# Kernel tuning notes

Hardware: AMD Instinct MI355X
Metric: run time of the kernel (lower is better)

The kernel has to match this reference:

```python
import jax, jax.numpy as jnp
import numpy as np

N, IN, D, H, C, G = 50000, 128, 64, 4, 10, 64
E_RAND = 800000
NEG_SLOPE = 0.2  # DGL GATConv default LeakyReLU slope


def setup_inputs() -> dict:
    key = jax.random.key(0)
    ks = jax.random.split(key, 20)
    h = jax.random.normal(ks[0], (N, IN), jnp.float32)
    # random edges + self-loops so every dst has at least one in-edge
    src = jnp.concatenate([jax.random.randint(ks[1], (E_RAND,), 0, N), jnp.arange(N)]).astype(jnp.int32)
    dst = jnp.concatenate([jax.random.randint(ks[2], (E_RAND,), 0, N), jnp.arange(N)]).astype(jnp.int32)
    graph_id = jnp.sort(jax.random.randint(ks[3], (N,), 0, G)).astype(jnp.int32)
    w = lambda k, s: jax.random.normal(k, s, jnp.float32) * 0.1
    return {
        "h": h, "src": src, "dst": dst, "graph_id": graph_id,
        "W0": w(ks[4], (IN, H * D)),    "al0": w(ks[5], (H, D)), "ar0": w(ks[6], (H, D)),
        "W1": w(ks[7], (H * D, H * D)), "al1": w(ks[8], (H, D)), "ar1": w(ks[9], (H, D)),
        "W2": w(ks[10], (H * D, H * D)), "al2": w(ks[11], (H, D)), "ar2": w(ks[12], (H, D)),
        "W3": w(ks[13], (H * D, D)),    "al3": w(ks[14], (1, D)), "ar3": w(ks[15], (1, D)),
        "fc1_w": w(ks[16], (D, D)), "fc1_b": jnp.zeros((D,), jnp.float32),
        "fc2_w": w(ks[17], (D, C)), "fc2_b": jnp.zeros((C,), jnp.float32),
    }


def gat_layer(x, W, al, ar, src, dst):
    """DGL GATConv: z=xW; e=LeakyReLU(a_l.z_src + a_r.z_dst); softmax over in-edges of dst; out=sum alpha*z_src."""
    nh, nd = al.shape
    z = (x @ W).reshape(N, nh, nd)                      # [N,H,D]
    el = jnp.sum(z * al, axis=-1)                       # [N,H]
    er = jnp.sum(z * ar, axis=-1)                       # [N,H]
    e = jax.nn.leaky_relu(el[src] + er[dst], NEG_SLOPE)  # [E,H]
    m = jax.ops.segment_max(e, dst, num_segments=N)     # per-dst max (stable softmax)
    ex = jnp.exp(e - m[dst])
    den = jax.ops.segment_sum(ex, dst, num_segments=N)
    alpha = ex / den[dst]                               # [E,H]
    msg = alpha[:, :, None] * z[src]                    # [E,H,D]
    return jax.ops.segment_sum(msg, dst, num_segments=N)  # [N,H,D]


def reference(h, src, dst, graph_id, W0, al0, ar0, W1, al1, ar1, W2, al2, ar2,
              W3, al3, ar3, fc1_w, fc1_b, fc2_w, fc2_b):
    x = jax.nn.relu(gat_layer(h, W0, al0, ar0, src, dst).reshape(N, -1))
    x = jax.nn.relu(gat_layer(x, W1, al1, ar1, src, dst).reshape(N, -1))
    x = jax.nn.relu(gat_layer(x, W2, al2, ar2, src, dst).reshape(N, -1))
    x = jax.nn.relu(gat_layer(x, W3, al3, ar3, src, dst).reshape(N, -1))  # [N,D] (1 head)
    # AvgPooling: mean node features per graph
    counts = jax.ops.segment_sum(jnp.ones((N,), x.dtype), graph_id, num_segments=G)
    pooled = jax.ops.segment_sum(x, graph_id, num_segments=G) / jnp.maximum(counts, 1.0)[:, None]
    y = jax.nn.elu(pooled @ fc1_w + fc1_b)
    y = y @ fc2_w + fc2_b
    return jax.nn.log_softmax(y, axis=0)  # original applies log_softmax over dim=0
```

## Files before the change

kernel.cpp:

```cpp
#include <hip/hip_runtime.h>
#include <hip/hip_bf16.h>
#include <math.h>

#define NN 50000
#define IN_F 128
#define DD 64
#define HH 4
#define CC 10
#define GG 64
#define NEG_SLOPE 0.2f

typedef __attribute__((ext_vector_type(8))) short bf16x8;
typedef __attribute__((ext_vector_type(4))) float f32x4;
typedef __attribute__((ext_vector_type(4))) unsigned short u16x4;

__device__ inline ushort f2bf(float f) {
    unsigned u = __float_as_uint(f);
    unsigned r = (u + 0x7fffu + ((u >> 16) & 1u)) >> 16;
    return (ushort)r;
}
__device__ inline float bf2f(ushort b) { return __uint_as_float(((unsigned)b) << 16); }

__device__ inline float wave_max(float v) {
#pragma unroll
    for (int o = 32; o > 0; o >>= 1) v = fmaxf(v, __shfl_xor(v, o));
    return v;
}
__device__ inline float wave_sum(float v) {
#pragma unroll
    for (int o = 32; o > 0; o >>= 1) v += __shfl_xor(v, o);
    return v;
}

__global__ void hist_kernel(const int* __restrict__ dst, int E, int* __restrict__ counts) {
    int i = blockIdx.x * blockDim.x + threadIdx.x;
    if (i < E) atomicAdd(&counts[dst[i]], 1);
}

__global__ __launch_bounds__(256) void scan_blk(const int* __restrict__ counts,
                                                int* __restrict__ excl,
                                                int* __restrict__ bsum, int n) {
    __shared__ int sh[256];
    int t = threadIdx.x;
    int i = blockIdx.x * 256 + t;
    int v = (i < n) ? counts[i] : 0;
    sh[t] = v;
    __syncthreads();
#pragma unroll
    for (int o = 1; o < 256; o <<= 1) {
        int u = (t >= o) ? sh[t - o] : 0;
        __syncthreads();
        sh[t] += u;
        __syncthreads();
    }
    if (i < n) excl[i] = sh[t] - v;
    if (t == 255) bsum[blockIdx.x] = sh[255];
}

__global__ __launch_bounds__(256) void scan_top(int* __restrict__ bsum, int nb) {
    __shared__ int sh[256];
    int t = threadIdx.x;
    int v = (t < nb) ? bsum[t] : 0;
    sh[t] = v;
    __syncthreads();
#pragma unroll
    for (int o = 1; o < 256; o <<= 1) {
        int u = (t >= o) ? sh[t - o] : 0;
        __syncthreads();
        sh[t] += u;
        __syncthreads();
    }
    if (t < nb) bsum[t] = sh[t] - v;
}

__global__ __launch_bounds__(256) void scan_fin(const int* __restrict__ excl,
                                                const int* __restrict__ bsum,
                                                int* __restrict__ row_ptr,
                                                int* __restrict__ fill, int n, int E) {
    int i = blockIdx.x * blockDim.x + threadIdx.x;
    if (i < n) {
        int r = excl[i] + bsum[i >> 8];
        row_ptr[i] = r;
        fill[i] = r;
    }
    if (i == 0) row_ptr[n] = E;
}

__global__ void scatter_kernel(const int* __restrict__ src, const int* __restrict__ dst,
                               int E, int* __restrict__ fill, int* __restrict__ col_src) {
    int i = blockIdx.x * blockDim.x + threadIdx.x;
    if (i < E) {
        int p = atomicAdd(&fill[dst[i]], 1);
        col_src[p] = src[i];
    }
}

__global__ void wconv_kernel(const float* __restrict__ W, int K, int N,
                             ushort* __restrict__ thi) {
    int i = blockIdx.x * blockDim.x + threadIdx.x;
    if (i >= K * N) return;
    int k = i / N, n = i - k * N;
    size_t o = ((size_t)(k >> 5) * N + n) * 32 + (k & 31);
    thi[o] = f2bf(W[i]);
}

template <int N, int H, bool AF32>
__global__ __launch_bounds__(256) void gemm_mfma_eler(
    const void* __restrict__ A0, const ushort* __restrict__ Alo,
    const ushort* __restrict__ Wthi,
    ushort* __restrict__ zt, const float* __restrict__ al, const float* __restrict__ ar,
    float* __restrict__ el, float* __restrict__ er, int M, int K) {
    constexpr int NT = N / 16;
    __shared__ ushort Bh[N][34];
    const int t = threadIdx.x;
    const int w = t >> 6, lane = t & 63;
    const int cl = lane & 15, g = lane >> 4;
    const int bm = blockIdx.x * 64;
    const int arow = bm + 16 * w + cl;
    const bool aval = arow < M;
    const size_t abase = (size_t)arow * K;
    const float* Af = (const float*)A0;
    const ushort* Ahi = (const ushort*)A0;

    f32x4 acc[NT];
#pragma unroll
    for (int nt = 0; nt < NT; ++nt) acc[nt] = (f32x4){0.f, 0.f, 0.f, 0.f};

    const int nkb = K >> 5;
    for (int kb = 0; kb < nkb; ++kb) {
        __syncthreads();
        if (t < N) {
            const float4* gsh = (const float4*)(Wthi + ((size_t)kb * N + t) * 32);
#pragma unroll
            for (int q = 0; q < 4; ++q) *(float4*)&Bh[t][q * 8] = gsh[q];
        }
        __syncthreads();
        bf16x8 a_hi = {0, 0, 0, 0, 0, 0, 0, 0};
        bf16x8 a_lo = {0, 0, 0, 0, 0, 0, 0, 0};
        if (aval) {
            if (AF32) {
                float4 f0 = *(const float4*)(Af + abase + kb * 32 + g * 8);
                float4 f1 = *(const float4*)(Af + abase + kb * 32 + g * 8 + 4);
                float fv[8] = {f0.x, f0.y, f0.z, f0.w, f1.x, f1.y, f1.z, f1.w};
#pragma unroll
                for (int q = 0; q < 8; ++q) {
                    ushort hb = f2bf(fv[q]);
                    a_hi[q] = (short)hb;
                    a_lo[q] = (short)f2bf(fv[q] - bf2f(hb));
                }
            } else {
                a_hi = *(const bf16x8*)(Ahi + abase + kb * 32 + g * 8);
                a_lo = *(const bf16x8*)(Alo + abase + kb * 32 + g * 8);
            }
        }
#pragma unroll
        for (int nt = 0; nt < NT; ++nt) {
            bf16x8 b_hi = *(const bf16x8*)&Bh[16 * nt + cl][g * 8];
            acc[nt] = __builtin_amdgcn_mfma_f32_16x16x32_bf16(a_hi, b_hi, acc[nt], 0, 0, 0);
            acc[nt] = __builtin_amdgcn_mfma_f32_16x16x32_bf16(a_lo, b_hi, acc[nt], 0, 0, 0);
        }
    }

    const int r0 = bm + 16 * w + 4 * g;
    if (H == 4) {
#pragma unroll
        for (int tt = 0; tt < 4; ++tt) {
#pragma unroll
            for (int j = 0; j < 4; ++j) {
                int r = r0 + j;
                if (r < M) {
                    u16x4 pv;
#pragma unroll
                    for (int h = 0; h < 4; ++h) pv[h] = f2bf(acc[4 * h + tt][j]);
                    *(u16x4*)&zt[(size_t)r * 256 + (16 * tt + cl) * 4] = pv;
                }
            }
        }
    } else {
#pragma unroll
        for (int nt = 0; nt < NT; ++nt) {
#pragma unroll
            for (int j = 0; j < 4; ++j) {
                int r = r0 + j;
                if (r < M) zt[(size_t)r * N + 16 * nt + cl] = f2bf(acc[nt][j]);
            }
        }
    }
#pragma unroll
    for (int h = 0; h < H; ++h) {
        float pl[4] = {0.f, 0.f, 0.f, 0.f};
        float pr[4] = {0.f, 0.f, 0.f, 0.f};
#pragma unroll
        for (int tt = 0; tt < 4; ++tt) {
            int nt = 4 * h + tt;
            float av = al[h * DD + 16 * tt + cl];
            float rv = ar[h * DD + 16 * tt + cl];
#pragma unroll
            for (int j = 0; j < 4; ++j) {
                pl[j] += acc[nt][j] * av;
                pr[j] += acc[nt][j] * rv;
            }
        }
#pragma unroll
        for (int j = 0; j < 4; ++j) {
#pragma unroll
            for (int o = 1; o < 16; o <<= 1) {
                pl[j] += __shfl_xor(pl[j], o);
                pr[j] += __shfl_xor(pr[j], o);
            }
        }
        if (cl == 0) {
#pragma unroll
            for (int j = 0; j < 4; ++j) {
                int r = r0 + j;
                if (r < M) {
                    el[(size_t)r * H + h] = pl[j];
                    er[(size_t)r * H + h] = pr[j];
                }
            }
        }
    }
}

template <int H, bool SPLIT>
__global__ __launch_bounds__(256) void agg_fused(const ushort* __restrict__ zt,
                                                 const float* __restrict__ el,
                                                 const float* __restrict__ er,
                                                 const int* __restrict__ row_ptr,
                                                 const int* __restrict__ col_src,
                                                 float* __restrict__ outf,
                                                 ushort* __restrict__ ohi,
                                                 ushort* __restrict__ olo) {
    __shared__ float alf[4][64][H];
    __shared__ int als[4][64];
    const int wid = threadIdx.x >> 6;
    const int lane = threadIdx.x & 63;
    int v = blockIdx.x * 4 + wid;
    if (v >= NN) return;
    int start = row_ptr[v], end = row_ptr[v + 1];
    int deg = end - start;
    float erd[H], acc[H];
#pragma unroll
    for (int h = 0; h < H; ++h) {
        erd[h] = er[(size_t)v * H + h];
        acc[h] = 0.f;
    }

    auto agg_chunk = [&](int cnt) {
        int j = 0;
        for (; j + 4 <= cnt; j += 4) {
            int s0 = als[wid][j + 0], s1 = als[wid][j + 1];
            int s2 = als[wid][j + 2], s3 = als[wid][j + 3];
            if (H == 4) {
                f32x4 a0 = *(const f32x4*)&alf[wid][j + 0][0];
                f32x4 a1 = *(const f32x4*)&alf[wid][j + 1][0];
                f32x4 a2 = *(const f32x4*)&alf[wid][j + 2][0];
                f32x4 a3 = *(const f32x4*)&alf[wid][j + 3][0];
                u16x4 z0 = *(const u16x4*)&zt[(size_t)s0 * 256 + lane * 4];
                u16x4 z1 = *(const u16x4*)&zt[(size_t)s1 * 256 + lane * 4];
                u16x4 z2 = *(const u16x4*)&zt[(size_t)s2 * 256 + lane * 4];
                u16x4 z3 = *(const u16x4*)&zt[(size_t)s3 * 256 + lane * 4];
#pragma unroll
                for (int h = 0; h < 4; ++h) {
                    acc[h] += a0[h] * bf2f(z0[h]);
                    acc[h] += a1[h] * bf2f(z1[h]);
                    acc[h] += a2[h] * bf2f(z2[h]);
                    acc[h] += a3[h] * bf2f(z3[h]);
                }
            } else {
                float a0 = alf[wid][j + 0][0], a1 = alf[wid][j + 1][0];
                float a2 = alf[wid][j + 2][0], a3 = alf[wid][j + 3][0];
                ushort z0 = zt[(size_t)s0 * 64 + lane];
                ushort z1 = zt[(size_t)s1 * 64 + lane];
                ushort z2 = zt[(size_t)s2 * 64 + lane];
                ushort z3 = zt[(size_t)s3 * 64 + lane];
                acc[0] += a0 * bf2f(z0);
                acc[0] += a1 * bf2f(z1);
                acc[0] += a2 * bf2f(z2);
                acc[0] += a3 * bf2f(z3);
            }
        }
        for (; j < cnt; ++j) {
            int s = als[wid][j];
            if (H == 4) {
                f32x4 a = *(const f32x4*)&alf[wid][j][0];
                u16x4 z = *(const u16x4*)&zt[(size_t)s * 256 + lane * 4];
#pragma unroll
                for (int h = 0; h < 4; ++h) acc[h] += a[h] * bf2f(z[h]);
            } else {
                acc[0] += alf[wid][j][0] * bf2f(zt[(size_t)s * 64 + lane]);
            }
        }
    };

    if (deg <= 64) {
        bool valid = lane < deg;
        int s = col_src[valid ? start + lane : start];
        als[wid][lane] = s;
        float e[H];
        if (H == 4) {
            f32x4 ev = *(const f32x4*)&el[(size_t)s * 4];
#pragma unroll
            for (int h = 0; h < 4; ++h) {
                float x = ev[h] + erd[h];
                x = (x >= 0.f) ? x : NEG_SLOPE * x;
                e[h] = valid ? x : -1e30f;
            }
        } else {
            float x = el[s] + erd[0];
            x = (x >= 0.f) ? x : NEG_SLOPE * x;
            e[0] = valid ? x : -1e30f;
        }
#pragma unroll
        for (int h = 0; h < H; ++h) {
            float m = wave_max(e[h]);
            float ex = valid ? __expf(e[h] - m) : 0.f;
            float den = wave_sum(ex);
            alf[wid][lane][h] = ex * (1.f / den);
        }
        __builtin_amdgcn_wave_barrier();
        agg_chunk(deg);
    } else {
        float m[H];
#pragma unroll
        for (int h = 0; h < H; ++h) m[h] = -1e30f;
        for (int base = start; base < end; base += 64) {
            int i = base + lane;
            bool valid = i < end;
            int s = col_src[valid ? i : start];
#pragma unroll
            for (int h = 0; h < H; ++h) {
                float x = el[(size_t)s * H + h] + erd[h];
                x = (x >= 0.f) ? x : NEG_SLOPE * x;
                m[h] = fmaxf(m[h], valid ? x : -1e30f);
            }
        }
        float den[H];
#pragma unroll
        for (int h = 0; h < H; ++h) {
            m[h] = wave_max(m[h]);
            den[h] = 0.f;
        }
        for (int base = start; base < end; base += 64) {
            int i = base + lane;
            bool valid = i < end;
            int s = col_src[valid ? i : start];
#pragma unroll
            for (int h = 0; h < H; ++h) {
                float x = el[(size_t)s * H + h] + erd[h];
                x = (x >= 0.f) ? x : NEG_SLOPE * x;
                den[h] += valid ? __expf(x - m[h]) : 0.f;
            }
        }
        float inv[H];
#pragma unroll
        for (int h = 0; h < H; ++h) inv[h] = 1.f / wave_sum(den[h]);
        for (int base = start; base < end; base += 64) {
            int i = base + lane;
            bool valid = i < end;
            int s = col_src[valid ? i : start];
            als[wid][lane] = s;
#pragma unroll
            for (int h = 0; h < H; ++h) {
                float x = el[(size_t)s * H + h] + erd[h];
                x = (x >= 0.f) ? x : NEG_SLOPE * x;
                alf[wid][lane][h] = valid ? __expf(x - m[h]) * inv[h] : 0.f;
            }
            __builtin_amdgcn_wave_barrier();
            int cnt = min(64, end - base);
            agg_chunk(cnt);
            __builtin_amdgcn_wave_barrier();
        }
    }

#pragma unroll
    for (int h = 0; h < H; ++h) {
        float r = acc[h];
        r = (r > 0.f) ? r : 0.f;
        size_t idx = (size_t)v * H * DD + h * DD + lane;
        if (SPLIT) {
            ushort hb = f2bf(r);
            ohi[idx] = hb;
            olo[idx] = f2bf(r - bf2f(hb));
        } else {
            outf[idx] = r;
        }
    }
}

__device__ inline int lower_bound_dev(const int* a, int n, int v) {
    int lo = 0, hi = n;
    while (lo < hi) {
        int mid = (lo + hi) >> 1;
        if (a[mid] < v) lo = mid + 1; else hi = mid;
    }
    return lo;
}

__global__ __launch_bounds__(256) void pool_kernel(const float* __restrict__ x,
                                                   const int* __restrict__ gid,
                                                   float* __restrict__ pooled,
                                                   float* __restrict__ gcnt) {
    int g = blockIdx.x;
    int start = lower_bound_dev(gid, NN, g);
    int end = lower_bound_dev(gid, NN, g + 1);
    int lane = threadIdx.x & 63;
    int w = threadIdx.x >> 6;
    float acc = 0.f;
    for (int i = start + w; i < end; i += 4) acc += x[(size_t)i * DD + lane];
    __shared__ float red[4][DD];
    red[w][lane] = acc;
    __syncthreads();
    if (w == 0) {
        float s = red[0][lane] + red[1][lane] + red[2][lane] + red[3][lane];
        pooled[g * DD + lane] = s;
        if (lane == 0) gcnt[g] = (float)(end - start);
    }
}

__global__ __launch_bounds__(64) void head_kernel(const float* __restrict__ pooled,
                                                  const float* __restrict__ gcnt,
                                                  const float* __restrict__ fc1w,
                                                  const float* __restrict__ fc1b,
                                                  const float* __restrict__ fc2w,
                                                  const float* __restrict__ fc2b,
                                                  float* __restrict__ out) {
    __shared__ float P[GG][DD + 1];
    __shared__ float Y1[GG][DD + 1];
    int g = threadIdx.x;
    float c = fmaxf(gcnt[g], 1.0f);
    for (int k = 0; k < DD; ++k) P[g][k] = pooled[g * DD + k] / c;
    __syncthreads();
    for (int j = 0; j < DD; ++j) {
        float s = fc1b[j];
        for (int k = 0; k < DD; ++k) s += P[g][k] * fc1w[k * DD + j];
        Y1[g][j] = (s > 0.f) ? s : expm1f(s);
    }
    __syncthreads();
    float y2[CC];
    for (int c2 = 0; c2 < CC; ++c2) {
        float s = fc2b[c2];
        for (int j = 0; j < DD; ++j) s += Y1[g][j] * fc2w[j * CC + c2];
        y2[c2] = s;
    }
    for (int c2 = 0; c2 < CC; ++c2) {
        float m = y2[c2];
#pragma unroll
        for (int o = 32; o > 0; o >>= 1) m = fmaxf(m, __shfl_xor(m, o));
        float sexp = __expf(y2[c2] - m);
#pragma unroll
        for (int o = 32; o > 0; o >>= 1) sexp += __shfl_xor(sexp, o);
        out[g * CC + c2] = y2[c2] - m - logf(sexp);
    }
}

extern "C" void kernel_launch(void* const* d_in, const int* in_sizes, int n_in,
                              void* d_out, int out_size, void* d_ws, size_t ws_size,
                              hipStream_t stream) {
    const float* h    = (const float*)d_in[0];
    const int* src    = (const int*)d_in[1];
    const int* dst    = (const int*)d_in[2];
    const int* gid    = (const int*)d_in[3];
    const float* W0   = (const float*)d_in[4];
    const float* al0  = (const float*)d_in[5];
    const float* ar0  = (const float*)d_in[6];
    const float* W1   = (const float*)d_in[7];
    const float* al1  = (const float*)d_in[8];
    const float* ar1  = (const float*)d_in[9];
    const float* W2   = (const float*)d_in[10];
    const float* al2  = (const float*)d_in[11];
    const float* ar2  = (const float*)d_in[12];
    const float* W3   = (const float*)d_in[13];
    const float* al3  = (const float*)d_in[14];
    const float* ar3  = (const float*)d_in[15];
    const float* fc1w = (const float*)d_in[16];
    const float* fc1b = (const float*)d_in[17];
    const float* fc2w = (const float*)d_in[18];
    const float* fc2b = (const float*)d_in[19];
    const int E = in_sizes[1];

    char* wsb = (char*)d_ws;
    size_t off = 0;
    auto alloc = [&](size_t bytes) -> void* {
        void* p = wsb + off;
        off = (off + bytes + 255) & ~(size_t)255;
        return p;
    };
    ushort* zt      = (ushort*)alloc((size_t)NN * 256 * 2);
    ushort* Ahi     = (ushort*)alloc((size_t)NN * 256 * 2);
    ushort* Alo     = (ushort*)alloc((size_t)NN * 256 * 2);
    float*  bufA    = (float*)alloc((size_t)NN * DD * 4);
    float*  el      = (float*)alloc((size_t)NN * HH * 4);
    float*  er      = (float*)alloc((size_t)NN * HH * 4);
    int*    counts  = (int*)alloc((size_t)NN * 4);
    int*    row_ptr = (int*)alloc((size_t)(NN + 1) * 4);
    int*    fill    = (int*)alloc((size_t)NN * 4);
    int*    excl    = (int*)alloc((size_t)NN * 4);
    int*    bsum    = (int*)alloc((size_t)256 * 4);
    int*    col_src = (int*)alloc((size_t)E * 4);
    float*  pooled  = (float*)alloc((size_t)GG * DD * 4);
    float*  gcnt    = (float*)alloc((size_t)GG * 4);
    ushort* w0h     = (ushort*)alloc((size_t)IN_F * 256 * 2);
    ushort* w1h     = (ushort*)alloc((size_t)256 * 256 * 2);
    ushort* w2h     = (ushort*)alloc((size_t)256 * 256 * 2);
    ushort* w3h     = (ushort*)alloc((size_t)256 * 64 * 2);

    hipMemsetAsync(counts, 0, (size_t)NN * 4, stream);
    int eg = (E + 255) / 256;
    const int nScanBlk = (NN + 255) / 256;
    hist_kernel<<<eg, 256, 0, stream>>>(dst, E, counts);
    scan_blk<<<nScanBlk, 256, 0, stream>>>(counts, excl, bsum, NN);
    scan_top<<<1, 256, 0, stream>>>(bsum, nScanBlk);
    scan_fin<<<nScanBlk, 256, 0, stream>>>(excl, bsum, row_ptr, fill, NN, E);
    scatter_kernel<<<eg, 256, 0, stream>>>(src, dst, E, fill, col_src);

    wconv_kernel<<<(IN_F * 256 + 255) / 256, 256, 0, stream>>>(W0, IN_F, 256, w0h);
    wconv_kernel<<<(256 * 256 + 255) / 256, 256, 0, stream>>>(W1, 256, 256, w1h);
    wconv_kernel<<<(256 * 256 + 255) / 256, 256, 0, stream>>>(W2, 256, 256, w2h);
    wconv_kernel<<<(256 * 64 + 255) / 256, 256, 0, stream>>>(W3, 256, 64, w3h);

    const int gemmGrid = (NN + 63) / 64;
    const int waveBlocks = (NN + 3) / 4;

    gemm_mfma_eler<256, 4, true><<<gemmGrid, 256, 0, stream>>>(h, nullptr, w0h, zt, al0, ar0, el, er, NN, IN_F);
    agg_fused<4, true><<<waveBlocks, 256, 0, stream>>>(zt, el, er, row_ptr, col_src, nullptr, Ahi, Alo);

    gemm_mfma_eler<256, 4, false><<<gemmGrid, 256, 0, stream>>>(Ahi, Alo, w1h, zt, al1, ar1, el, er, NN, 256);
    agg_fused<4, true><<<waveBlocks, 256, 0, stream>>>(zt, el, er, row_ptr, col_src, nullptr, Ahi, Alo);

    gemm_mfma_eler<256, 4, false><<<gemmGrid, 256, 0, stream>>>(Ahi, Alo, w2h, zt, al2, ar2, el, er, NN, 256);
    agg_fused<4, true><<<waveBlocks, 256, 0, stream>>>(zt, el, er, row_ptr, col_src, nullptr, Ahi, Alo);

    gemm_mfma_eler<64, 1, false><<<gemmGrid, 256, 0, stream>>>(Ahi, Alo, w3h, zt, al3, ar3, el, er, NN, 256);
    agg_fused<1, false><<<waveBlocks, 256, 0, stream>>>(zt, el, er, row_ptr, col_src, bufA, nullptr, nullptr);

    pool_kernel<<<GG, 256, 0, stream>>>(bufA, gid, pooled, gcnt);
    head_kernel<<<1, 64, 0, stream>>>(pooled, gcnt, fc1w, fc1b, fc2w, fc2b, (float*)d_out);
}
```

Measured before the change: 627.1 us.

## Store z features as FP8 E4M3 for gathers and read GEMM weights directly

In the three 4-head layers, the GEMM now writes z as software-encoded FP8 E4M3 bytes instead of bf16. The aggregation kernel decodes them, which halves the bytes moved by the random per-edge gather. The GEMM also drops its shared-memory staging of the weight tile and the two barriers per K-step, loading B fragments straight from global memory or cache. The cost is lower precision in the messages, which may exceed tolerance, plus extra ALU work to encode and decode FP8.

```diff
diff --git a/kernel.cpp b/kernel.cpp
--- a/kernel.cpp
+++ b/kernel.cpp
@@ -12,7 +12,6 @@
 
 typedef __attribute__((ext_vector_type(8))) short bf16x8;
 typedef __attribute__((ext_vector_type(4))) float f32x4;
-typedef __attribute__((ext_vector_type(4))) unsigned short u16x4;
 
 __device__ inline ushort f2bf(float f) {
     unsigned u = __float_as_uint(f);
@@ -20,6 +19,26 @@
     return (ushort)r;
 }
 __device__ inline float bf2f(ushort b) { return __uint_as_float(((unsigned)b) << 16); }
+
+__device__ inline unsigned f2fp8(float f) {
+    float a = fabsf(f);
+    a = fminf(a, 448.f);
+    unsigned s = (__float_as_uint(f) >> 31) << 7;
+    unsigned bits;
+    if (a < 0.015625f) {
+        bits = (unsigned)__float2int_rn(a * 512.f);
+    } else {
+        unsigned u = __float_as_uint(a);
+        u += 0x7ffffu + ((u >> 20) & 1u);
+        bits = (u >> 20) - (120u << 3);
+        bits = min(bits, 0x7Eu);
+    }
+    return s | bits;
+}
+__device__ inline float fp82f(unsigned b) {
+    unsigned u = ((b & 0x80u) << 24) | ((b & 0x7fu) << 20);
+    return __uint_as_float(u) * 0x1p120f;
+}
 
 __device__ inline float wave_max(float v) {
 #pragma unroll
@@ -108,10 +127,9 @@
 __global__ __launch_bounds__(256) void gemm_mfma_eler(
     const void* __restrict__ A0, const ushort* __restrict__ Alo,
     const ushort* __restrict__ Wthi,
-    ushort* __restrict__ zt, const float* __restrict__ al, const float* __restrict__ ar,
+    void* __restrict__ ztv, const float* __restrict__ al, const float* __restrict__ ar,
     float* __restrict__ el, float* __restrict__ er, int M, int K) {
     constexpr int NT = N / 16;
-    __shared__ ushort Bh[N][34];
     const int t = threadIdx.x;
     const int w = t >> 6, lane = t & 63;
     const int cl = lane & 15, g = lane >> 4;
@@ -128,13 +146,6 @@
 
     const int nkb = K >> 5;
     for (int kb = 0; kb < nkb; ++kb) {
-        __syncthreads();
-        if (t < N) {
-            const float4* gsh = (const float4*)(Wthi + ((size_t)kb * N + t) * 32);
-#pragma unroll
-            for (int q = 0; q < 4; ++q) *(float4*)&Bh[t][q * 8] = gsh[q];
-        }
-        __syncthreads();
         bf16x8 a_hi = {0, 0, 0, 0, 0, 0, 0, 0};
         bf16x8 a_lo = {0, 0, 0, 0, 0, 0, 0, 0};
         if (aval) {
@@ -153,9 +164,10 @@
                 a_lo = *(const bf16x8*)(Alo + abase + kb * 32 + g * 8);
             }
         }
+        const ushort* wb = Wthi + (size_t)kb * N * 32;
 #pragma unroll
         for (int nt = 0; nt < NT; ++nt) {
-            bf16x8 b_hi = *(const bf16x8*)&Bh[16 * nt + cl][g * 8];
+            bf16x8 b_hi = *(const bf16x8*)(wb + (16 * nt + cl) * 32 + g * 8);
             acc[nt] = __builtin_amdgcn_mfma_f32_16x16x32_bf16(a_hi, b_hi, acc[nt], 0, 0, 0);
             acc[nt] = __builtin_amdgcn_mfma_f32_16x16x32_bf16(a_lo, b_hi, acc[nt], 0, 0, 0);
         }
@@ -163,20 +175,21 @@
 
     const int r0 = bm + 16 * w + 4 * g;
     if (H == 4) {
+        unsigned char* zf8 = (unsigned char*)ztv;
 #pragma unroll
         for (int tt = 0; tt < 4; ++tt) {
 #pragma unroll
             for (int j = 0; j < 4; ++j) {
                 int r = r0 + j;
                 if (r < M) {
-                    u16x4 pv;
-#pragma unroll
-                    for (int h = 0; h < 4; ++h) pv[h] = f2bf(acc[4 * h + tt][j]);
-                    *(u16x4*)&zt[(size_t)r * 256 + (16 * tt + cl) * 4] = pv;
+                    unsigned pw = f2fp8(acc[tt][j]) | (f2fp8(acc[4 + tt][j]) << 8) |
+                                  (f2fp8(acc[8 + tt][j]) << 16) | (f2fp8(acc[12 + tt][j]) << 24);
+                    *(unsigned*)&zf8[(size_t)r * 256 + (16 * tt + cl) * 4] = pw;
                 }
             }
         }
     } else {
+        ushort* zt = (ushort*)ztv;
 #pragma unroll
         for (int nt = 0; nt < NT; ++nt) {
 #pragma unroll
@@ -223,7 +236,7 @@
 }
 
 template <int H, bool SPLIT>
-__global__ __launch_bounds__(256) void agg_fused(const ushort* __restrict__ zt,
+__global__ __launch_bounds__(256) void agg_fused(const void* __restrict__ ztv,
                                                  const float* __restrict__ el,
                                                  const float* __restrict__ er,
                                                  const int* __restrict__ row_ptr,
@@ -233,6 +246,8 @@
                                                  ushort* __restrict__ olo) {
     __shared__ float alf[4][64][H];
     __shared__ int als[4][64];
+    const unsigned char* zf8 = (const unsigned char*)ztv;
+    const ushort* zt16 = (const ushort*)ztv;
     const int wid = threadIdx.x >> 6;
     const int lane = threadIdx.x & 63;
     int v = blockIdx.x * 4 + wid;
@@ -256,24 +271,24 @@
                 f32x4 a1 = *(const f32x4*)&alf[wid][j + 1][0];
                 f32x4 a2 = *(const f32x4*)&alf[wid][j + 2][0];
                 f32x4 a3 = *(const f32x4*)&alf[wid][j + 3][0];
-                u16x4 z0 = *(const u16x4*)&zt[(size_t)s0 * 256 + lane * 4];
-                u16x4 z1 = *(const u16x4*)&zt[(size_t)s1 * 256 + lane * 4];
-                u16x4 z2 = *(const u16x4*)&zt[(size_t)s2 * 256 + lane * 4];
-                u16x4 z3 = *(const u16x4*)&zt[(size_t)s3 * 256 + lane * 4];
+                unsigned z0 = *(const unsigned*)&zf8[(size_t)s0 * 256 + lane * 4];
+                unsigned z1 = *(const unsigned*)&zf8[(size_t)s1 * 256 + lane * 4];
+                unsigned z2 = *(const unsigned*)&zf8[(size_t)s2 * 256 + lane * 4];
+                unsigned z3 = *(const unsigned*)&zf8[(size_t)s3 * 256 + lane * 4];
 #pragma unroll
                 for (int h = 0; h < 4; ++h) {
-                    acc[h] += a0[h] * bf2f(z0[h]);
-                    acc[h] += a1[h] * bf2f(z1[h]);
-                    acc[h] += a2[h] * bf2f(z2[h]);
-                    acc[h] += a3[h] * bf2f(z3[h]);
+                    acc[h] += a0[h] * fp82f((z0 >> (8 * h)) & 0xffu);
+                    acc[h] += a1[h] * fp82f((z1 >> (8 * h)) & 0xffu);
+                    acc[h] += a2[h] * fp82f((z2 >> (8 * h)) & 0xffu);
+                    acc[h] += a3[h] * fp82f((z3 >> (8 * h)) & 0xffu);
                 }
             } else {
                 float a0 = alf[wid][j + 0][0], a1 = alf[wid][j + 1][0];
                 float a2 = alf[wid][j + 2][0], a3 = alf[wid][j + 3][0];
-                ushort z0 = zt[(size_t)s0 * 64 + lane];
-                ushort z1 = zt[(size_t)s1 * 64 + lane];
-                ushort z2 = zt[(size_t)s2 * 64 + lane];
-                ushort z3 = zt[(size_t)s3 * 64 + lane];
+                ushort z0 = zt16[(size_t)s0 * 64 + lane];
+                ushort z1 = zt16[(size_t)s1 * 64 + lane];
+                ushort z2 = zt16[(size_t)s2 * 64 + lane];
+                ushort z3 = zt16[(size_t)s3 * 64 + lane];
                 acc[0] += a0 * bf2f(z0);
                 acc[0] += a1 * bf2f(z1);
                 acc[0] += a2 * bf2f(z2);
@@ -284,11 +299,11 @@
             int s = als[wid][j];
             if (H == 4) {
                 f32x4 a = *(const f32x4*)&alf[wid][j][0];
-                u16x4 z = *(const u16x4*)&zt[(size_t)s * 256 + lane * 4];
-#pragma unroll
-                for (int h = 0; h < 4; ++h) acc[h] += a[h] * bf2f(z[h]);
+                unsigned z = *(const unsigned*)&zf8[(size_t)s * 256 + lane * 4];
+#pragma unroll
+                for (int h = 0; h < 4; ++h) acc[h] += a[h] * fp82f((z >> (8 * h)) & 0xffu);
             } else {
-                acc[0] += alf[wid][j][0] * bf2f(zt[(size_t)s * 64 + lane]);
+                acc[0] += alf[wid][j][0] * bf2f(zt16[(size_t)s * 64 + lane]);
             }
         }
     };
@@ -486,7 +501,8 @@
         off = (off + bytes + 255) & ~(size_t)255;
         return p;
     };
-    ushort* zt      = (ushort*)alloc((size_t)NN * 256 * 2);
+    unsigned char* zf8 = (unsigned char*)alloc((size_t)NN * 256);
+    ushort* zt16    = (ushort*)alloc((size_t)NN * DD * 2);
     ushort* Ahi     = (ushort*)alloc((size_t)NN * 256 * 2);
     ushort* Alo     = (ushort*)alloc((size_t)NN * 256 * 2);
     float*  bufA    = (float*)alloc((size_t)NN * DD * 4);
@@ -522,17 +538,17 @@
     const int gemmGrid = (NN + 63) / 64;
     const int waveBlocks = (NN + 3) / 4;
 
-    gemm_mfma_eler<256, 4, true><<<gemmGrid, 256, 0, stream>>>(h, nullptr, w0h, zt, al0, ar0, el, er, NN, IN_F);
-    agg_fused<4, true><<<waveBlocks, 256, 0, stream>>>(zt, el, er, row_ptr, col_src, nullptr, Ahi, Alo);
-
-    gemm_mfma_eler<256, 4, false><<<gemmGrid, 256, 0, stream>>>(Ahi, Alo, w1h, zt, al1, ar1, el, er, NN, 256);
-    agg_fused<4, true><<<waveBlocks, 256, 0, stream>>>(zt, el, er, row_ptr, col_src, nullptr, Ahi, Alo);
-
-    gemm_mfma_eler<256, 4, false><<<gemmGrid, 256, 0, stream>>>(Ahi, Alo, w2h, zt, al2, ar2, el, er, NN, 256);
-    agg_fused<4, true><<<waveBlocks, 256, 0, stream>>>(zt, el, er, row_ptr, col_src, nullptr, Ahi, Alo);
-
-    gemm_mfma_eler<64, 1, false><<<gemmGrid, 256, 0, stream>>>(Ahi, Alo, w3h, zt, al3, ar3, el, er, NN, 256);
-    agg_fused<1, false><<<waveBlocks, 256, 0, stream>>>(zt, el, er, row_ptr, col_src, bufA, nullptr, nullptr);
+    gemm_mfma_eler<256, 4, true><<<gemmGrid, 256, 0, stream>>>(h, nullptr, w0h, zf8, al0, ar0, el, er, NN, IN_F);
+    agg_fused<4, true><<<waveBlocks, 256, 0, stream>>>(zf8, el, er, row_ptr, col_src, nullptr, Ahi, Alo);
+
+    gemm_mfma_eler<256, 4, false><<<gemmGrid, 256, 0, stream>>>(Ahi, Alo, w1h, zf8, al1, ar1, el, er, NN, 256);
+    agg_fused<4, true><<<waveBlocks, 256, 0, stream>>>(zf8, el, er, row_ptr, col_src, nullptr, Ahi, Alo);
+
+    gemm_mfma_eler<256, 4, false><<<gemmGrid, 256, 0, stream>>>(Ahi, Alo, w2h, zf8, al2, ar2, el, er, NN, 256);
+    agg_fused<4, true><<<waveBlocks, 256, 0, stream>>>(zf8, el, er, row_ptr, col_src, nullptr, Ahi, Alo);
+
+    gemm_mfma_eler<64, 1, false><<<gemmGrid, 256, 0, stream>>>(Ahi, Alo, w3h, zt16, al3, ar3, el, er, NN, 256);
+    agg_fused<1, false><<<waveBlocks, 256, 0, stream>>>(zt16, el, er, row_ptr, col_src, bufA, nullptr, nullptr);
 
     pool_kernel<<<GG, 256, 0, stream>>>(bufA, gid, pooled, gcnt);
     head_kernel<<<1, 64, 0, stream>>>(pooled, gcnt, fc1w, fc1b, fc2w, fc2b, (float*)d_out);
```

Result: slower. 783.4 us (+24.9%).
